# Kernel tuning notes

Hardware: AMD Instinct MI355X
Metric: run time of the kernel (lower is better)

Reference implementation:

```python
import jax, jax.numpy as jnp
import numpy as np

B, T_ENC, ENC_D = 32, 256, 512
T_DEC, MEL, R = 500, 80, 2
PRE = 256
ATTN_D, ATTN_RNN, DEC_RNN = 128, 1024, 1024
FILTERS, KSIZE = 32, 31
PAD = (KSIZE - 1) // 2


def setup_inputs() -> dict:
    key = jax.random.key(0)
    ks = jax.random.split(key, 32)
    n = lambda i, shape, s=0.05: jax.random.normal(ks[i], shape, dtype=jnp.float32) * s
    inp = {
        'encoder_outputs': jax.random.normal(ks[0], (B, T_ENC, ENC_D), dtype=jnp.float32),
        'inputs': jax.random.normal(ks[1], (B, T_DEC, MEL), dtype=jnp.float32),
        'memory_lengths': jax.random.randint(ks[2], (B,), T_ENC // 2, T_ENC + 1, dtype=jnp.int32),
        # prenet
        'W1': n(3, (PRE, MEL)), 'b1': jnp.zeros((PRE,), jnp.float32),
        'W2': n(4, (PRE, PRE)), 'b2': jnp.zeros((PRE,), jnp.float32),
        # memory layer
        'Wm': n(5, (ATTN_D, ENC_D)),
        # attention LSTMCell (input = PRE + ENC_D)
        'Wih_a': n(6, (4 * ATTN_RNN, PRE + ENC_D)), 'Whh_a': n(7, (4 * ATTN_RNN, ATTN_RNN)),
        'bih_a': jnp.zeros((4 * ATTN_RNN,), jnp.float32), 'bhh_a': jnp.zeros((4 * ATTN_RNN,), jnp.float32),
        # location-sensitive attention
        'Wq': n(8, (ATTN_D, ATTN_RNN)),
        'conv_w': n(9, (FILTERS, 1, KSIZE)), 'conv_b': jnp.zeros((FILTERS,), jnp.float32),
        'WL': n(10, (ATTN_D, FILTERS)),
        'v': n(11, (1, ATTN_D)),
        # decoder LSTMCell (input = ATTN_RNN + ENC_D)
        'Wih_d': n(12, (4 * DEC_RNN, ATTN_RNN + ENC_D)), 'Whh_d': n(13, (4 * DEC_RNN, DEC_RNN)),
        'bih_d': jnp.zeros((4 * DEC_RNN,), jnp.float32), 'bhh_d': jnp.zeros((4 * DEC_RNN,), jnp.float32),
        # projections (input = DEC_RNN + ENC_D)
        'Wmel': n(14, (MEL * R, DEC_RNN + ENC_D)), 'bmel': jnp.zeros((MEL * R,), jnp.float32),
        'Wstop': n(15, (1, DEC_RNN + ENC_D)), 'bstop': jnp.zeros((1,), jnp.float32),
    }
    return inp


def _lstm_cell(x, h, c, Wih, Whh, bih, bhh):
    gates = x @ Wih.T + bih + h @ Whh.T + bhh
    i, f, g, o = jnp.split(gates, 4, axis=-1)
    c = jax.nn.sigmoid(f) * c + jax.nn.sigmoid(i) * jnp.tanh(g)
    h = jax.nn.sigmoid(o) * jnp.tanh(c)
    return h, c


def _decoder(encoder_outputs, inputs, memory_lengths,
             W1, b1, W2, b2, Wm, Wih_a, Whh_a, bih_a, bhh_a,
             Wq, conv_w, conv_b, WL, v,
             Wih_d, Whh_d, bih_d, bhh_d, Wmel, bmel, Wstop, bstop):
    bsz = encoder_outputs.shape[0]
    t_enc = encoder_outputs.shape[1]
    processed_memory = encoder_outputs @ Wm.T  # (B, T_enc, attn_d)
    mask = jnp.arange(t_enc)[None, :] >= memory_lengths[:, None]  # True = padded

    n_steps = T_DEC // R
    # teacher-forced input frame per step: go frame, then last frame of each group
    tf = jnp.transpose(inputs[:, R - 1:T_DEC - 1:R, :], (1, 0, 2))  # (N-1, B, MEL)
    frames = jnp.concatenate([jnp.zeros((1, bsz, MEL), inputs.dtype), tf], axis=0)  # (N, B, MEL)

    def step(carry, frame):
        attn_h, attn_c, dec_h, dec_c, ctx, cum = carry
        # prenet (dropout disabled for deterministic reference / eval)
        x = jax.nn.relu(frame @ W1.T + b1)
        x = jax.nn.relu(x @ W2.T + b2)
        # attention LSTM cell
        attn_h, attn_c = _lstm_cell(jnp.concatenate([x, ctx], -1), attn_h, attn_c,
                                    Wih_a, Whh_a, bih_a, bhh_a)
        # location-sensitive energies
        pq = attn_h @ Wq.T  # (B, attn_d)
        loc = jax.lax.conv_general_dilated(
            cum[:, None, :], conv_w, window_strides=(1,), padding=[(PAD, PAD)],
            dimension_numbers=('NCH', 'OIH', 'NCH')) + conv_b[None, :, None]  # (B, F, T)
        ploc = jnp.transpose(loc, (0, 2, 1)) @ WL.T  # (B, T, attn_d)
        e = jnp.tanh(pq[:, None, :] + processed_memory + ploc) @ v[0]  # (B, T)
        e = jnp.where(mask, -1e9, e)
        align = jax.nn.softmax(e, axis=1)
        cum = cum + align
        ctx = jnp.einsum('bt,btd->bd', align, encoder_outputs)
        # decoder LSTM cell
        dec_h, dec_c = _lstm_cell(jnp.concatenate([attn_h, ctx], -1), dec_h, dec_c,
                                  Wih_d, Whh_d, bih_d, bhh_d)
        proj_in = jnp.concatenate([dec_h, ctx], -1)
        mel = (proj_in @ Wmel.T + bmel).reshape(bsz, R, MEL)
        stop = jax.nn.sigmoid(proj_in @ Wstop.T + bstop)  # (B, 1)
        return (attn_h, attn_c, dec_h, dec_c, ctx, cum), (mel, stop, align)

    z = lambda d: jnp.zeros((bsz, d), encoder_outputs.dtype)
    carry0 = (z(ATTN_RNN), z(ATTN_RNN), z(DEC_RNN), z(DEC_RNN), z(ENC_D),
              jnp.zeros((bsz, t_enc), encoder_outputs.dtype))
    _, (mels, stops, aligns) = jax.lax.scan(step, carry0, frames)
    mel_outputs = jnp.transpose(mels, (1, 0, 2, 3)).reshape(bsz, n_steps * R, MEL)
    stop_tokens = jnp.repeat(jnp.transpose(stops[:, :, 0]), R, axis=1)  # (B, N*R)
    attn_scores = jnp.transpose(aligns, (1, 0, 2))  # (B, N, T_enc)
    return mel_outputs, stop_tokens, attn_scores


def reference(encoder_outputs, inputs, memory_lengths,
              W1, b1, W2, b2, Wm, Wih_a, Whh_a, bih_a, bhh_a,
              Wq, conv_w, conv_b, WL, v,
              Wih_d, Whh_d, bih_d, bhh_d, Wmel, bmel, Wstop, bstop):
    return _decoder(encoder_outputs, inputs, memory_lengths,
                    W1, b1, W2, b2, Wm, Wih_a, Whh_a, bih_a, bhh_a,
                    Wq, conv_w, conv_b, WL, v,
                    Wih_d, Whh_d, bih_d, bhh_d, Wmel, bmel, Wstop, bstop)
```

## Files before the change

### kernel.cpp

```cpp
#include <hip/hip_runtime.h>
#include <cstdio>

static constexpr int cB = 32, cTENC = 256, cENCD = 512, cTDEC = 500, cMEL = 80,
    cNSTEP = 250, cPRE = 256, cAD = 128, cAR = 1024, cDR = 1024, cFLT = 32,
    cKSZ = 31, cPADC = 15, cNG = 4096;
static constexpr int cKA = cPRE + cENCD + cAR;
static constexpr int cKD = cAR + cENCD + cDR;
static constexpr int cKM = cDR + cENCD;
static constexpr int cNMP = 192;
static constexpr int cNSA = 14;
static constexpr int cNSD = 16;

typedef unsigned short ushortT;
typedef unsigned int uintT;
typedef unsigned long long ullT;

static constexpr size_t MEL_OFF = 0;
static constexpr size_t STOP_OFF = (size_t)cB * cTDEC * cMEL;
static constexpr size_t ATT_OFF = STOP_OFF + (size_t)cB * cTDEC;

static constexpr size_t WS_WATB = 0;
static constexpr size_t WS_WDTB = WS_WATB + (size_t)cKA * cNG / 2;
static constexpr size_t WS_WMT  = WS_WDTB + (size_t)cKD * cNG / 2;
static constexpr size_t WS_WQT  = WS_WMT  + (size_t)cKM * cNMP;
static constexpr size_t WS_WMTR = WS_WQT  + (size_t)cAR * cAD;
static constexpr size_t WS_PM   = WS_WMTR + (size_t)cENCD * cAD;
static constexpr size_t WS_XPRE = WS_PM   + (size_t)cB * cTENC * cAD;
static constexpr size_t WS_XA   = WS_XPRE + (size_t)cNSTEP * cPRE * cB;
static constexpr size_t WS_XD   = WS_XA   + (size_t)2 * cKA * cB;
static constexpr size_t WS_CA   = WS_XD   + (size_t)cKD * cB;
static constexpr size_t WS_CD   = WS_CA   + (size_t)cB * cAR;
static constexpr size_t WS_CUM  = WS_CD   + (size_t)cB * cDR;
static constexpr size_t WS_CTR  = WS_CUM  + (size_t)cB * cTENC;
static constexpr size_t WS_GA   = WS_CTR  + 16;
static constexpr size_t WS_GD   = WS_GA   + (size_t)cB * cNSA * cNG;
static constexpr size_t WS_PROJ = WS_GD   + (size_t)cB * cNSD * cNG;
static constexpr size_t WS_TOTAL = WS_PROJ + (size_t)cNSTEP * cKM * cB;
static constexpr size_t WS_X1   = WS_GA;

struct Args {
  const float *enc, *inputs;
  const int *mlen;
  const float *W1, *b1, *W2, *b2, *Wm;
  const float *Wih_a, *Whh_a, *bih_a, *bhh_a;
  const float *Wq, *conv_w, *conv_b, *WL, *v;
  const float *Wih_d, *Whh_d, *bih_d, *bhh_d;
  const float *Wmel, *bmel, *Wstop, *bstop;
  float *out;
  float *ws;
};

union SharedU {
  float xs[(160 + 8) * 32];
  struct {
    float h[cAR];
    float pq[cAD];
    float cumext[cTENC + 2 * cPADC];
    float eparts[2][cTENC];
    float e[cTENC];
    float sred[16];
    float loc[cFLT * 257];
    float wl[cAD * 33];
    float cw[cFLT * cKSZ];
    float vv[cAD];
  } attn;
  float melred[cB][164];
};

__device__ __forceinline__ float ld_sc(const float* p) {
  return __hip_atomic_load(p, __ATOMIC_RELAXED, __HIP_MEMORY_SCOPE_AGENT);
}
__device__ __forceinline__ void st_sc(float* p, float v) {
  __hip_atomic_store(p, v, __ATOMIC_RELAXED, __HIP_MEMORY_SCOPE_AGENT);
}
__device__ __forceinline__ float2 ld_sc2(const float2* p) {
  ullT u = __hip_atomic_load((const ullT*)p, __ATOMIC_RELAXED, __HIP_MEMORY_SCOPE_AGENT);
  float2 r;
  r.x = __uint_as_float((uintT)u);
  r.y = __uint_as_float((uintT)(u >> 32));
  return r;
}
__device__ __forceinline__ void st_sc2(float2* p, float x, float y) {
  ullT u = (ullT)__float_as_uint(x) | ((ullT)__float_as_uint(y) << 32);
  __hip_atomic_store((ullT*)p, u, __ATOMIC_RELAXED, __HIP_MEMORY_SCOPE_AGENT);
}

__device__ __forceinline__ void gbar(uintT* ctr, uintT target) {
  __syncthreads();
  if (threadIdx.x == 0) {
    __hip_atomic_fetch_add(ctr, 1u, __ATOMIC_RELAXED, __HIP_MEMORY_SCOPE_AGENT);
    while (__hip_atomic_load(ctr, __ATOMIC_RELAXED, __HIP_MEMORY_SCOPE_AGENT) < target) {
      __builtin_amdgcn_s_sleep(4);
    }
  }
  __syncthreads();
}

__device__ __forceinline__ float sigm_f(float x) { return 1.f / (1.f + __expf(-x)); }
__device__ __forceinline__ float tanh_f(float x) {
  float e = __expf(2.f * x);
  return 1.f - 2.f / (e + 1.f);
}

template <int KSPAN, int NS>
static __device__ void gemv_bf16(const ushortT* __restrict__ WT,
                                 const float* __restrict__ xT,
                                 float* __restrict__ part,
                                 int cb, int k0, int slot, float* __restrict__ xs) {
  const int tid = threadIdx.x;
  {
    const float2* src = (const float2*)(xT + (size_t)k0 * cB);
    float2* dst = (float2*)xs;
    for (int i = tid; i < KSPAN * 16; i += 512) dst[i] = ld_sc2(src + i);
  }
  __syncthreads();
  const int cq = tid & 63, bq = tid >> 6;
  const int col0 = cb * 512 + cq * 8;
  const ushortT* wp = WT + (size_t)k0 * cNG + col0;
  const float4* xp = (const float4*)xs + bq;
  float acc[8][4];
#pragma unroll
  for (int c = 0; c < 8; ++c)
#pragma unroll
    for (int j = 0; j < 4; ++j) acc[c][j] = 0.f;

  constexpr int PF = 8;
  uint4 wbuf[PF];
  float4 xbuf[PF];
#pragma unroll
  for (int i = 0; i < PF; ++i) {
    wbuf[i] = *(const uint4*)(wp + (size_t)i * cNG);
    xbuf[i] = xp[(size_t)i * 8];
  }
  for (int kb = 0; kb < KSPAN; kb += PF) {
#pragma unroll
    for (int i = 0; i < PF; ++i) {
      const uint4 w = wbuf[i];
      const float4 x4 = xbuf[i];
      const size_t kn = (size_t)(kb + i + PF);
      wbuf[i] = *(const uint4*)(wp + kn * cNG);
      xbuf[i] = xp[kn * 8];
      float wf[8];
      wf[0] = __uint_as_float(w.x << 16);
      wf[1] = __uint_as_float(w.x & 0xFFFF0000u);
      wf[2] = __uint_as_float(w.y << 16);
      wf[3] = __uint_as_float(w.y & 0xFFFF0000u);
      wf[4] = __uint_as_float(w.z << 16);
      wf[5] = __uint_as_float(w.z & 0xFFFF0000u);
      wf[6] = __uint_as_float(w.w << 16);
      wf[7] = __uint_as_float(w.w & 0xFFFF0000u);
      const float xv[4] = {x4.x, x4.y, x4.z, x4.w};
#pragma unroll
      for (int c = 0; c < 8; ++c)
#pragma unroll
        for (int j = 0; j < 4; ++j) acc[c][j] = fmaf(wf[c], xv[j], acc[c][j]);
    }
  }
  const int b0 = bq * 4;
#pragma unroll
  for (int j = 0; j < 4; ++j) {
    float2* dst = (float2*)&part[(((size_t)(b0 + j)) * NS + slot) * cNG + col0];
    st_sc2(dst + 0, acc[0][j], acc[1][j]);
    st_sc2(dst + 1, acc[2][j], acc[3][j]);
    st_sc2(dst + 2, acc[4][j], acc[5][j]);
    st_sc2(dst + 3, acc[6][j], acc[7][j]);
  }
  __syncthreads();
}

static __device__ void dec_cell(const Args& a, float* ws, int b, int s) {
  const int tid = threadIdx.x;
  const float* gd = ws + WS_GD + (size_t)b * cNSD * cNG;
  for (int h = tid; h < cDR; h += 512) {
    float g4[4];
#pragma unroll
    for (int gi = 0; gi < 4; ++gi) {
      const int n = gi * cDR + h;
      float sm = a.bih_d[n] + a.bhh_d[n];
#pragma unroll
      for (int p = 0; p < cNSD; ++p) sm += ld_sc(gd + (size_t)p * cNG + n);
      g4[gi] = sm;
    }
    const float co = ld_sc(ws + WS_CD + (size_t)b * cDR + h);
    const float cn = sigm_f(g4[1]) * co + sigm_f(g4[0]) * tanh_f(g4[2]);
    const float hn = sigm_f(g4[3]) * tanh_f(cn);
    st_sc(ws + WS_CD + (size_t)b * cDR + h, cn);
    st_sc(ws + WS_XD + (size_t)(cAR + cENCD + h) * cB + b, hn);
    st_sc(ws + WS_PROJ + ((size_t)s * cKM + h) * cB + b, hn);
  }
}

static __device__ void attn_wg(const Args& a, float* ws, int b, int t,
                               float* __restrict__ xa2, SharedU& sh) {
  const int tid = threadIdx.x;
  const float* ga = ws + WS_GA + (size_t)b * cNSA * cNG;
  for (int h = tid; h < cAR; h += 512) {
    float g4[4];
#pragma unroll
    for (int gi = 0; gi < 4; ++gi) {
      const int n = gi * cAR + h;
      float s = a.bih_a[n] + a.bhh_a[n];
#pragma unroll
      for (int p = 0; p < cNSA; ++p) s += ld_sc(ga + (size_t)p * cNG + n);
      g4[gi] = s;
    }
    const float co = ld_sc(ws + WS_CA + (size_t)b * cAR + h);
    const float cn = sigm_f(g4[1]) * co + sigm_f(g4[0]) * tanh_f(g4[2]);
    const float hn = sigm_f(g4[3]) * tanh_f(cn);
    st_sc(ws + WS_CA + (size_t)b * cAR + h, cn);
    sh.attn.h[h] = hn;
    st_sc(xa2 + (size_t)(cPRE + cENCD + h) * cB + b, hn);
    st_sc(ws + WS_XD + (size_t)h * cB + b, hn);
  }
  __syncthreads();
  {
    const int d = tid & 127, kc = tid >> 7;
    float acc = 0.f;
    const float* wq = ws + WS_WQT;
    const int k0 = kc * 256;
    for (int k = k0; k < k0 + 256; ++k) acc = fmaf(sh.attn.h[k], wq[(size_t)k * cAD + d], acc);
    sh.attn.loc[kc * 128 + d] = acc;
  }
  for (int i = tid; i < cAD * 33; i += 512) {
    const int dd = i / 33, f = i - dd * 33;
    sh.attn.wl[i] = (f < cFLT) ? a.WL[dd * cFLT + f] : 0.f;
  }
  for (int i = tid; i < cFLT * cKSZ; i += 512) sh.attn.cw[i] = a.conv_w[i];
  if (tid < cAD) sh.attn.vv[tid] = a.v[tid];
  if (tid < cTENC) sh.attn.cumext[cPADC + tid] = ld_sc(ws + WS_CUM + (size_t)b * cTENC + tid);
  if (tid < 2 * cPADC) sh.attn.cumext[tid < cPADC ? tid : cTENC + tid] = 0.f;
  __syncthreads();
  if (tid < cAD)
    sh.attn.pq[tid] = sh.attn.loc[tid] + sh.attn.loc[128 + tid] +
                      sh.attn.loc[256 + tid] + sh.attn.loc[384 + tid];
  __syncthreads();
  for (int i = tid; i < cFLT * cTENC; i += 512) {
    const int f = i >> 8, te = i & 255;
    float s = a.conv_b[f];
#pragma unroll
    for (int j = 0; j < cKSZ; ++j) s = fmaf(sh.attn.cumext[te + j], sh.attn.cw[f * cKSZ + j], s);
    sh.attn.loc[f * 257 + te] = s;
  }
  __syncthreads();
  {
    const int d = tid & 127, tq = tid >> 7, wv = tid >> 6;
    float wlr[cFLT];
#pragma unroll
    for (int f = 0; f < cFLT; ++f) wlr[f] = sh.attn.wl[d * 33 + f];
    const float pqd = sh.attn.pq[d], vd = sh.attn.vv[d];
    const float* pmb = ws + WS_PM + (size_t)b * cTENC * cAD;
    for (int tt = 0; tt < cTENC / 4; ++tt) {
      const int te = tt * 4 + tq;
      float s = pqd + pmb[(size_t)te * cAD + d];
#pragma unroll
      for (int f = 0; f < cFLT; ++f) s = fmaf(sh.attn.loc[f * 257 + te], wlr[f], s);
      float p = tanh_f(s) * vd;
#pragma unroll
      for (int off = 32; off > 0; off >>= 1) p += __shfl_xor(p, off, 64);
      if ((tid & 63) == 0) sh.attn.eparts[wv & 1][te] = p;
    }
  }
  __syncthreads();
  const int mlen = a.mlen[b];
  if (tid < cTENC) {
    float ev = sh.attn.eparts[0][tid] + sh.attn.eparts[1][tid];
    if (tid >= mlen) ev = -1e9f;
    sh.attn.e[tid] = ev;
  }
  __syncthreads();
  const int wv = tid >> 6;
  {
    float xv = sh.attn.e[tid & 255];
#pragma unroll
    for (int off = 32; off > 0; off >>= 1) xv = fmaxf(xv, __shfl_xor(xv, off, 64));
    if ((tid & 63) == 0) sh.attn.sred[wv] = xv;
  }
  __syncthreads();
  float m = sh.attn.sred[0];
#pragma unroll
  for (int i = 1; i < 8; ++i) m = fmaxf(m, sh.attn.sred[i]);
  const float pex = (tid < cTENC) ? __expf(sh.attn.e[tid] - m) : 0.f;
  {
    float sv = pex;
#pragma unroll
    for (int off = 32; off > 0; off >>= 1) sv += __shfl_xor(sv, off, 64);
    if ((tid & 63) == 0) sh.attn.sred[8 + wv] = sv;
  }
  __syncthreads();
  float ssum = 0.f;
#pragma unroll
  for (int i = 0; i < 8; ++i) ssum += sh.attn.sred[8 + i];
  const float rs = 1.f / ssum;
  if (tid < cTENC) {
    const float al = pex * rs;
    sh.attn.e[tid] = al;
    a.out[ATT_OFF + ((size_t)b * cNSTEP + t) * cTENC + tid] = al;
    st_sc(ws + WS_CUM + (size_t)b * cTENC + tid, sh.attn.cumext[cPADC + tid] + al);
  }
  __syncthreads();
  {
    const int k = tid;
    float acc = 0.f;
    const float* encb = a.enc + (size_t)b * cTENC * cENCD + k;
    for (int te = 0; te < cTENC; ++te) acc = fmaf(sh.attn.e[te], encb[(size_t)te * cENCD], acc);
    st_sc(xa2 + (size_t)(cPRE + k) * cB + b, acc);
    st_sc(ws + WS_XD + (size_t)(cAR + k) * cB + b, acc);
    st_sc(ws + WS_PROJ + ((size_t)t * cKM + cDR + k) * cB + b, acc);
  }
}

static __device__ void mel_proj(const Args& a, float* ws, SharedU& sh) {
  const int tid = threadIdx.x;
  const int c = tid & 255, sub = tid >> 8;
  for (int t = blockIdx.x; t < cNSTEP; t += gridDim.x) {
    float acc[cB];
#pragma unroll
    for (int b = 0; b < cB; ++b) acc[b] = 0.f;
    if (c < 161) {
      const float* wmt = ws + WS_WMT;
      const float* xr0 = ws + WS_PROJ + (size_t)t * cKM * cB;
      const int k0 = sub * 768;
      for (int k = k0; k < k0 + 768; ++k) {
        const float w = wmt[(size_t)k * cNMP + c];
        const float* xr = xr0 + (size_t)k * cB;
#pragma unroll
        for (int b = 0; b < cB; ++b) acc[b] = fmaf(w, ld_sc(xr + b), acc[b]);
      }
    }
    __syncthreads();
    if (sub == 1 && c < 161) {
#pragma unroll
      for (int b = 0; b < cB; ++b) sh.melred[b][c] = acc[b];
    }
    __syncthreads();
    if (sub == 0 && c < 161) {
      if (c < 160) {
        const int fr = c / 80, mm = c % 80;
        const float bm = a.bmel[c];
#pragma unroll
        for (int b = 0; b < cB; ++b) {
          const float val = acc[b] + sh.melred[b][c] + bm;
          a.out[MEL_OFF + ((size_t)b * cTDEC + (2 * t + fr)) * cMEL + mm] = val;
        }
      } else {
        const float bs = a.bstop[0];
#pragma unroll
        for (int b = 0; b < cB; ++b) {
          const float sp = sigm_f(acc[b] + sh.melred[b][c] + bs);
          a.out[STOP_OFF + (size_t)b * cTDEC + 2 * t] = sp;
          a.out[STOP_OFF + (size_t)b * cTDEC + 2 * t + 1] = sp;
        }
      }
    }
    __syncthreads();
  }
}

__device__ __forceinline__ ushortT f2b(float f) {
  const uintT u = __float_as_uint(f);
  return (ushortT)((u + 0x7FFFu + ((u >> 16) & 1u)) >> 16);
}

__global__ void k_transpose(const float* __restrict__ src, float* __restrict__ dst,
                            int N, int K, int dpitch) {
  __shared__ float tile[64][65];
  const int tkn = K >> 6;
  const int tk = blockIdx.x % tkn, tn = blockIdx.x / tkn;
  const int c = threadIdx.x & 63, r4 = threadIdx.x >> 6;
  const int n0 = tn << 6, k0 = tk << 6;
#pragma unroll
  for (int rr = 0; rr < 16; ++rr) {
    const int r = r4 * 16 + rr;
    tile[r][c] = src[(size_t)(n0 + r) * K + k0 + c];
  }
  __syncthreads();
#pragma unroll
  for (int rr = 0; rr < 16; ++rr) {
    const int r = r4 * 16 + rr;
    dst[(size_t)(k0 + r) * dpitch + n0 + c] = tile[c][r];
  }
}

__global__ void k_transpose_b16(const float* __restrict__ src, ushortT* __restrict__ dst,
                                int N, int K, int dpitch) {
  __shared__ float tile[64][65];
  const int tkn = K >> 6;
  const int tk = blockIdx.x % tkn, tn = blockIdx.x / tkn;
  const int c = threadIdx.x & 63, r4 = threadIdx.x >> 6;
  const int n0 = tn << 6, k0 = tk << 6;
#pragma unroll
  for (int rr = 0; rr < 16; ++rr) {
    const int r = r4 * 16 + rr;
    tile[r][c] = src[(size_t)(n0 + r) * K + k0 + c];
  }
  __syncthreads();
#pragma unroll
  for (int rr = 0; rr < 16; ++rr) {
    const int r = r4 * 16 + rr;
    dst[(size_t)(k0 + r) * dpitch + n0 + c] = f2b(tile[c][r]);
  }
}

__global__ void k_prep_small(Args a) {
  const size_t i = (size_t)blockIdx.x * blockDim.x + threadIdx.x;
  if (i < 16) ((uintT*)(a.ws + WS_CTR))[i] = 0u;
  if (i >= (size_t)cKM * cNMP) return;
  const int k = (int)(i / cNMP), c = (int)(i % cNMP);
  a.ws[WS_WMT + i] = (c < 160) ? a.Wmel[(size_t)c * cKM + k]
                               : (c == 160 ? a.Wstop[k] : 0.f);
}

__global__ void k_prenet1(Args a) {
  const size_t i = (size_t)blockIdx.x * blockDim.x + threadIdx.x;
  if (i >= (size_t)cNSTEP * cB * cPRE) return;
  const int j = i & 255, b = (i >> 8) & 31, n = (int)(i >> 13);
  float acc = a.b1[j];
  if (n > 0) {
    const float* fr = a.inputs + ((size_t)b * cTDEC + (2 * n - 1)) * cMEL;
    for (int k = 0; k < cMEL; ++k) acc = fmaf(fr[k], a.W1[j * cMEL + k], acc);
  }
  a.ws[WS_X1 + i] = fmaxf(acc, 0.f);
}

__global__ void k_prenet2(Args a) {
  const size_t i = (size_t)blockIdx.x * blockDim.x + threadIdx.x;
  if (i >= (size_t)cNSTEP * cPRE * cB) return;
  const int b = i & 31, j = (i >> 5) & 255, n = (int)(i >> 13);
  float acc = a.b2[j];
  const float* x1 = a.ws + WS_X1 + ((size_t)n * cB + b) * cPRE;
  for (int k = 0; k < cPRE; ++k) acc = fmaf(x1[k], a.W2[j * cPRE + k], acc);
  a.ws[WS_XPRE + i] = fmaxf(acc, 0.f);
}

__global__ void k_pm(Args a) {
  const size_t i = (size_t)blockIdx.x * blockDim.x + threadIdx.x;
  if (i >= (size_t)cB * cTENC * cAD) return;
  const int d = i & 127, tt = (i >> 7) & 255, b = (int)(i >> 15);
  float acc = 0.f;
  const float* er = a.enc + ((size_t)b * cTENC + tt) * cENCD;
  const float* wt = a.ws + WS_WMTR;
  for (int k = 0; k < cENCD; ++k) acc = fmaf(er[k], wt[(size_t)k * cAD + d], acc);
  a.ws[WS_PM + i] = acc;
}

__global__ void __launch_bounds__(512, 1) k_loop(Args a) {
  __shared__ SharedU sh;
  float* ws = a.ws;
  uintT* ctr = (uintT*)(ws + WS_CTR);
  const ushortT* watb = (const ushortT*)(ws + WS_WATB);
  const ushortT* wdtb = (const ushortT*)(ws + WS_WDTB);
  const int wg = blockIdx.x;
  const int tid = threadIdx.x;
  uintT ph = 0;

  float* xa0 = ws + WS_XA;
  if (wg < 32) {
    const int b = wg;
    for (int i = tid; i < cTENC; i += 512) st_sc(ws + WS_CUM + (size_t)b * cTENC + i, 0.f);
    for (int i = tid; i < cAR; i += 512) st_sc(ws + WS_CA + (size_t)b * cAR + i, 0.f);
  } else if (wg < 64) {
    const int b = wg - 32;
    for (int i = tid; i < cDR; i += 512) st_sc(ws + WS_CD + (size_t)b * cDR + i, 0.f);
  } else if (wg < 80) {
    const int i = (wg - 64) * 512 + tid;
    st_sc(xa0 + i, ld_sc(ws + WS_XPRE + i));
  } else if (wg < 176) {
    const int i = (wg - 80) * 512 + tid;
    st_sc(xa0 + (size_t)cPRE * cB + i, 0.f);
  } else if (wg < 240) {
    const int i = (wg - 176) * 512 + tid;
    st_sc(ws + WS_XD + (size_t)(cAR + cENCD) * cB + i, 0.f);
  }
  ++ph; gbar(ctr, ph * 256u);

  for (int t = 0; t <= cNSTEP; ++t) {
    const float* xa = ws + WS_XA + (size_t)(t & 1) * cKA * cB;
    float* xa2 = ws + WS_XA + (size_t)((t + 1) & 1) * cKA * cB;
    if (wg < 112) {
      if (t < cNSTEP) {
        const int s = wg >> 3, cb = wg & 7;
        gemv_bf16<128, cNSA>(watb, xa, ws + WS_GA, cb, s * 128, s, sh.xs);
      }
    } else if (wg < 240) {
      if (t >= 1) {
        const int i = wg - 112, s = i >> 3, cb = i & 7;
        gemv_bf16<160, cNSD>(wdtb, ws + WS_XD, ws + WS_GD, cb, s * 160, s, sh.xs);
      }
    }
    ++ph; gbar(ctr, ph * 256u);
    if (wg < 32) {
      if (t < cNSTEP) attn_wg(a, ws, wg, t, xa2, sh);
    } else if (wg < 64) {
      if (t >= 1) dec_cell(a, ws, wg - 32, t - 1);
    } else if (wg < 80) {
      if (t + 1 < cNSTEP) {
        const int i = (wg - 64) * 512 + tid;
        st_sc(xa2 + i, ld_sc(ws + WS_XPRE + (size_t)(t + 1) * cPRE * cB + i));
      }
    }
    ++ph; gbar(ctr, ph * 256u);
  }
  mel_proj(a, ws, sh);
}

extern "C" void kernel_launch(void* const* d_in, const int* in_sizes, int n_in,
                              void* d_out, int out_size, void* d_ws, size_t ws_size,
                              hipStream_t stream) {
  (void)in_sizes; (void)n_in; (void)out_size;
  Args a;
  a.enc = (const float*)d_in[0];
  a.inputs = (const float*)d_in[1];
  a.mlen = (const int*)d_in[2];
  a.W1 = (const float*)d_in[3];  a.b1 = (const float*)d_in[4];
  a.W2 = (const float*)d_in[5];  a.b2 = (const float*)d_in[6];
  a.Wm = (const float*)d_in[7];
  a.Wih_a = (const float*)d_in[8];  a.Whh_a = (const float*)d_in[9];
  a.bih_a = (const float*)d_in[10]; a.bhh_a = (const float*)d_in[11];
  a.Wq = (const float*)d_in[12];
  a.conv_w = (const float*)d_in[13]; a.conv_b = (const float*)d_in[14];
  a.WL = (const float*)d_in[15];     a.v = (const float*)d_in[16];
  a.Wih_d = (const float*)d_in[17];  a.Whh_d = (const float*)d_in[18];
  a.bih_d = (const float*)d_in[19];  a.bhh_d = (const float*)d_in[20];
  a.Wmel = (const float*)d_in[21];   a.bmel = (const float*)d_in[22];
  a.Wstop = (const float*)d_in[23];  a.bstop = (const float*)d_in[24];
  a.out = (float*)d_out;
  a.ws = (float*)d_ws;

  if (ws_size < WS_TOTAL * sizeof(float)) {
    fprintf(stderr, "kernel_launch: ws too small: need %zu bytes, have %zu\n",
            WS_TOTAL * sizeof(float), ws_size);
    return;
  }

  float* ws = a.ws;
  ushortT* watb = (ushortT*)(ws + WS_WATB);
  ushortT* wdtb = (ushortT*)(ws + WS_WDTB);
  k_transpose_b16<<<dim3((768 / 64) * (4096 / 64)), dim3(256), 0, stream>>>(
      a.Wih_a, watb, 4096, 768, cNG);
  k_transpose_b16<<<dim3((1024 / 64) * (4096 / 64)), dim3(256), 0, stream>>>(
      a.Whh_a, watb + (size_t)768 * cNG, 4096, 1024, cNG);
  k_transpose_b16<<<dim3((1536 / 64) * (4096 / 64)), dim3(256), 0, stream>>>(
      a.Wih_d, wdtb, 4096, 1536, cNG);
  k_transpose_b16<<<dim3((1024 / 64) * (4096 / 64)), dim3(256), 0, stream>>>(
      a.Whh_d, wdtb + (size_t)1536 * cNG, 4096, 1024, cNG);
  k_transpose<<<dim3((1024 / 64) * (128 / 64)), dim3(256), 0, stream>>>(
      a.Wq, ws + WS_WQT, 128, 1024, cAD);
  k_transpose<<<dim3((512 / 64) * (128 / 64)), dim3(256), 0, stream>>>(
      a.Wm, ws + WS_WMTR, 128, 512, cAD);

  k_prep_small<<<dim3((cKM * cNMP + 255) / 256), dim3(256), 0, stream>>>(a);
  k_prenet1<<<dim3(8000), dim3(256), 0, stream>>>(a);
  k_prenet2<<<dim3(8000), dim3(256), 0, stream>>>(a);
  k_pm<<<dim3(4096), dim3(256), 0, stream>>>(a);

  void* params[] = { (void*)&a };
  hipError_t err = hipLaunchCooperativeKernel((const void*)k_loop, dim3(256), dim3(512),
                                              params, 0, stream);
  if (err != hipSuccess) {
    fprintf(stderr, "kernel_launch: cooperative launch failed: %s\n",
            hipGetErrorString(err));
  }
}
```

Before: 39.10 ms.

## Keep per-block LSTM weight slices resident in LDS across all decoder steps

Each GEMV block now loads its bf16 weight slice (128 or 132 rows × 512 columns) into dynamic shared memory once, then reuses it for all 250 steps. Only the few extra decoder rows are streamed from global memory. This removes the per-step global re-read of the LSTM weights. Activation buffers change to batch-major layout, attention moves to blocks 240-255 (each handles two batch rows), and the global barrier is split across 8 padded counters to reduce atomic contention. The cost is about 158KB of LDS per block and serialized attention work on 16 blocks.

```diff
diff --git a/kernel.cpp b/kernel.cpp
--- a/kernel.cpp
+++ b/kernel.cpp
@@ -10,6 +10,9 @@
 static constexpr int cNMP = 192;
 static constexpr int cNSA = 14;
 static constexpr int cNSD = 16;
+static constexpr int cRDA = 128;
+static constexpr int cRDD = 132;
+static constexpr int cDYN = 158208;
 
 typedef unsigned short ushortT;
 typedef unsigned int uintT;
@@ -32,7 +35,7 @@
 static constexpr size_t WS_CD   = WS_CA   + (size_t)cB * cAR;
 static constexpr size_t WS_CUM  = WS_CD   + (size_t)cB * cDR;
 static constexpr size_t WS_CTR  = WS_CUM  + (size_t)cB * cTENC;
-static constexpr size_t WS_GA   = WS_CTR  + 16;
+static constexpr size_t WS_GA   = WS_CTR  + 128;
 static constexpr size_t WS_GD   = WS_GA   + (size_t)cB * cNSA * cNG;
 static constexpr size_t WS_PROJ = WS_GD   + (size_t)cB * cNSD * cNG;
 static constexpr size_t WS_TOTAL = WS_PROJ + (size_t)cNSTEP * cKM * cB;
@@ -50,21 +53,17 @@
   float *ws;
 };
 
-union SharedU {
-  float xs[(160 + 8) * 32];
-  struct {
-    float h[cAR];
-    float pq[cAD];
-    float cumext[cTENC + 2 * cPADC];
-    float eparts[2][cTENC];
-    float e[cTENC];
-    float sred[16];
-    float loc[cFLT * 257];
-    float wl[cAD * 33];
-    float cw[cFLT * cKSZ];
-    float vv[cAD];
-  } attn;
-  float melred[cB][164];
+struct AttnSh {
+  float h[cAR];
+  float pq[cAD];
+  float cumext[cTENC + 2 * cPADC];
+  float eparts[2][cTENC];
+  float e[cTENC];
+  float sred[16];
+  float loc[cFLT * 257];
+  float wl[cAD * 33];
+  float cw[cFLT * cKSZ];
+  float vv[cAD];
 };
 
 __device__ __forceinline__ float ld_sc(const float* p) {
@@ -72,26 +71,22 @@
 }
 __device__ __forceinline__ void st_sc(float* p, float v) {
   __hip_atomic_store(p, v, __ATOMIC_RELAXED, __HIP_MEMORY_SCOPE_AGENT);
-}
-__device__ __forceinline__ float2 ld_sc2(const float2* p) {
-  ullT u = __hip_atomic_load((const ullT*)p, __ATOMIC_RELAXED, __HIP_MEMORY_SCOPE_AGENT);
-  float2 r;
-  r.x = __uint_as_float((uintT)u);
-  r.y = __uint_as_float((uintT)(u >> 32));
-  return r;
 }
 __device__ __forceinline__ void st_sc2(float2* p, float x, float y) {
   ullT u = (ullT)__float_as_uint(x) | ((ullT)__float_as_uint(y) << 32);
   __hip_atomic_store((ullT*)p, u, __ATOMIC_RELAXED, __HIP_MEMORY_SCOPE_AGENT);
 }
 
-__device__ __forceinline__ void gbar(uintT* ctr, uintT target) {
-  __syncthreads();
-  if (threadIdx.x == 0) {
-    __hip_atomic_fetch_add(ctr, 1u, __ATOMIC_RELAXED, __HIP_MEMORY_SCOPE_AGENT);
-    while (__hip_atomic_load(ctr, __ATOMIC_RELAXED, __HIP_MEMORY_SCOPE_AGENT) < target) {
-      __builtin_amdgcn_s_sleep(4);
-    }
+__device__ __forceinline__ void gbar(uintT* ctrs, uintT ph) {
+  __syncthreads();
+  if (threadIdx.x == 0)
+    __hip_atomic_fetch_add(ctrs + (blockIdx.x & 7) * 16, 1u,
+                           __ATOMIC_RELAXED, __HIP_MEMORY_SCOPE_AGENT);
+  if (threadIdx.x < 8) {
+    const uintT target = ph * 32u;
+    while (__hip_atomic_load(ctrs + threadIdx.x * 16, __ATOMIC_RELAXED,
+                             __HIP_MEMORY_SCOPE_AGENT) < target)
+      __builtin_amdgcn_s_sleep(8);
   }
   __syncthreads();
 }
@@ -102,70 +97,76 @@
   return 1.f - 2.f / (e + 1.f);
 }
 
-template <int KSPAN, int NS>
-static __device__ void gemv_bf16(const ushortT* __restrict__ WT,
-                                 const float* __restrict__ xT,
-                                 float* __restrict__ part,
-                                 int cb, int k0, int slot, float* __restrict__ xs) {
+__device__ __forceinline__ void fma8x4(float (&acc)[8][4], const uint4 w, const float4 x4) {
+  float wf[8];
+  wf[0] = __uint_as_float(w.x << 16);
+  wf[1] = __uint_as_float(w.x & 0xFFFF0000u);
+  wf[2] = __uint_as_float(w.y << 16);
+  wf[3] = __uint_as_float(w.y & 0xFFFF0000u);
+  wf[4] = __uint_as_float(w.z << 16);
+  wf[5] = __uint_as_float(w.z & 0xFFFF0000u);
+  wf[6] = __uint_as_float(w.w << 16);
+  wf[7] = __uint_as_float(w.w & 0xFFFF0000u);
+  const float xv[4] = {x4.x, x4.y, x4.z, x4.w};
+#pragma unroll
+  for (int c = 0; c < 8; ++c)
+#pragma unroll
+    for (int j = 0; j < 4; ++j) acc[c][j] = fmaf(wf[c], xv[j], acc[c][j]);
+}
+
+static __device__ void preload_w(uint4* dst, const ushortT* src, int rows) {
+  const int tid = threadIdx.x;
+  for (int i = tid; i < rows * 64; i += 512) {
+    const int r = i >> 6, u = i & 63;
+    dst[i] = *(const uint4*)(src + (size_t)r * cNG + u * 8);
+  }
+}
+
+template <int KSPAN, int RD, int NS>
+static __device__ void gemv_lds(const ushortT* __restrict__ wlds,
+                                const ushortT* __restrict__ wstream,
+                                const float* __restrict__ xT, int xstride,
+                                float* __restrict__ part,
+                                int col0, int slot, float* __restrict__ xs) {
   const int tid = threadIdx.x;
   {
-    const float2* src = (const float2*)(xT + (size_t)k0 * cB);
-    float2* dst = (float2*)xs;
-    for (int i = tid; i < KSPAN * 16; i += 512) dst[i] = ld_sc2(src + i);
+    const int b = tid >> 4, kt = tid & 15;
+    const float* src = xT + (size_t)b * xstride;
+    for (int k = kt; k < KSPAN; k += 16) xs[k * 36 + b] = ld_sc(src + k);
   }
   __syncthreads();
   const int cq = tid & 63, bq = tid >> 6;
-  const int col0 = cb * 512 + cq * 8;
-  const ushortT* wp = WT + (size_t)k0 * cNG + col0;
-  const float4* xp = (const float4*)xs + bq;
+  const ushortT* wl = wlds + cq * 8;
+  const float* xp = xs + bq * 4;
   float acc[8][4];
 #pragma unroll
   for (int c = 0; c < 8; ++c)
 #pragma unroll
     for (int j = 0; j < 4; ++j) acc[c][j] = 0.f;
-
-  constexpr int PF = 8;
-  uint4 wbuf[PF];
-  float4 xbuf[PF];
-#pragma unroll
-  for (int i = 0; i < PF; ++i) {
-    wbuf[i] = *(const uint4*)(wp + (size_t)i * cNG);
-    xbuf[i] = xp[(size_t)i * 8];
-  }
-  for (int kb = 0; kb < KSPAN; kb += PF) {
-#pragma unroll
-    for (int i = 0; i < PF; ++i) {
-      const uint4 w = wbuf[i];
-      const float4 x4 = xbuf[i];
-      const size_t kn = (size_t)(kb + i + PF);
-      wbuf[i] = *(const uint4*)(wp + kn * cNG);
-      xbuf[i] = xp[kn * 8];
-      float wf[8];
-      wf[0] = __uint_as_float(w.x << 16);
-      wf[1] = __uint_as_float(w.x & 0xFFFF0000u);
-      wf[2] = __uint_as_float(w.y << 16);
-      wf[3] = __uint_as_float(w.y & 0xFFFF0000u);
-      wf[4] = __uint_as_float(w.z << 16);
-      wf[5] = __uint_as_float(w.z & 0xFFFF0000u);
-      wf[6] = __uint_as_float(w.w << 16);
-      wf[7] = __uint_as_float(w.w & 0xFFFF0000u);
-      const float xv[4] = {x4.x, x4.y, x4.z, x4.w};
-#pragma unroll
-      for (int c = 0; c < 8; ++c)
-#pragma unroll
-        for (int j = 0; j < 4; ++j) acc[c][j] = fmaf(wf[c], xv[j], acc[c][j]);
+#pragma unroll 4
+  for (int k = 0; k < RD; ++k) {
+    const uint4 w = *(const uint4*)(wl + (size_t)k * 512);
+    const float4 x4 = *(const float4*)(xp + k * 36);
+    fma8x4(acc, w, x4);
+  }
+  if (RD < KSPAN) {
+    const ushortT* wg2 = wstream + cq * 8;
+#pragma unroll 4
+    for (int k = RD; k < KSPAN; ++k) {
+      const uint4 w = *(const uint4*)(wg2 + (size_t)k * cNG);
+      const float4 x4 = *(const float4*)(xp + k * 36);
+      fma8x4(acc, w, x4);
     }
   }
   const int b0 = bq * 4;
 #pragma unroll
   for (int j = 0; j < 4; ++j) {
-    float2* dst = (float2*)&part[(((size_t)(b0 + j)) * NS + slot) * cNG + col0];
+    float2* dst = (float2*)&part[(((size_t)(b0 + j)) * NS + slot) * cNG + col0 + cq * 8];
     st_sc2(dst + 0, acc[0][j], acc[1][j]);
     st_sc2(dst + 1, acc[2][j], acc[3][j]);
     st_sc2(dst + 2, acc[4][j], acc[5][j]);
     st_sc2(dst + 3, acc[6][j], acc[7][j]);
   }
-  __syncthreads();
 }
 
 static __device__ void dec_cell(const Args& a, float* ws, int b, int s) {
@@ -185,13 +186,13 @@
     const float cn = sigm_f(g4[1]) * co + sigm_f(g4[0]) * tanh_f(g4[2]);
     const float hn = sigm_f(g4[3]) * tanh_f(cn);
     st_sc(ws + WS_CD + (size_t)b * cDR + h, cn);
-    st_sc(ws + WS_XD + (size_t)(cAR + cENCD + h) * cB + b, hn);
-    st_sc(ws + WS_PROJ + ((size_t)s * cKM + h) * cB + b, hn);
+    st_sc(ws + WS_XD + (size_t)b * cKD + (cAR + cENCD) + h, hn);
+    st_sc(ws + WS_PROJ + ((size_t)s * cB + b) * cKM + h, hn);
   }
 }
 
 static __device__ void attn_wg(const Args& a, float* ws, int b, int t,
-                               float* __restrict__ xa2, SharedU& sh) {
+                               float* __restrict__ xa2, AttnSh& sh) {
   const int tid = threadIdx.x;
   const float* ga = ws + WS_GA + (size_t)b * cNSA * cNG;
   for (int h = tid; h < cAR; h += 512) {
@@ -208,9 +209,9 @@
     const float cn = sigm_f(g4[1]) * co + sigm_f(g4[0]) * tanh_f(g4[2]);
     const float hn = sigm_f(g4[3]) * tanh_f(cn);
     st_sc(ws + WS_CA + (size_t)b * cAR + h, cn);
-    sh.attn.h[h] = hn;
-    st_sc(xa2 + (size_t)(cPRE + cENCD + h) * cB + b, hn);
-    st_sc(ws + WS_XD + (size_t)h * cB + b, hn);
+    sh.h[h] = hn;
+    st_sc(xa2 + (size_t)b * cKA + (cPRE + cENCD) + h, hn);
+    st_sc(ws + WS_XD + (size_t)b * cKD + h, hn);
   }
   __syncthreads();
   {
@@ -218,98 +219,98 @@
     float acc = 0.f;
     const float* wq = ws + WS_WQT;
     const int k0 = kc * 256;
-    for (int k = k0; k < k0 + 256; ++k) acc = fmaf(sh.attn.h[k], wq[(size_t)k * cAD + d], acc);
-    sh.attn.loc[kc * 128 + d] = acc;
+    for (int k = k0; k < k0 + 256; ++k) acc = fmaf(sh.h[k], wq[(size_t)k * cAD + d], acc);
+    sh.loc[kc * 128 + d] = acc;
   }
   for (int i = tid; i < cAD * 33; i += 512) {
     const int dd = i / 33, f = i - dd * 33;
-    sh.attn.wl[i] = (f < cFLT) ? a.WL[dd * cFLT + f] : 0.f;
-  }
-  for (int i = tid; i < cFLT * cKSZ; i += 512) sh.attn.cw[i] = a.conv_w[i];
-  if (tid < cAD) sh.attn.vv[tid] = a.v[tid];
-  if (tid < cTENC) sh.attn.cumext[cPADC + tid] = ld_sc(ws + WS_CUM + (size_t)b * cTENC + tid);
-  if (tid < 2 * cPADC) sh.attn.cumext[tid < cPADC ? tid : cTENC + tid] = 0.f;
+    sh.wl[i] = (f < cFLT) ? a.WL[dd * cFLT + f] : 0.f;
+  }
+  for (int i = tid; i < cFLT * cKSZ; i += 512) sh.cw[i] = a.conv_w[i];
+  if (tid < cAD) sh.vv[tid] = a.v[tid];
+  if (tid < cTENC) sh.cumext[cPADC + tid] = ld_sc(ws + WS_CUM + (size_t)b * cTENC + tid);
+  if (tid < 2 * cPADC) sh.cumext[tid < cPADC ? tid : cTENC + tid] = 0.f;
   __syncthreads();
   if (tid < cAD)
-    sh.attn.pq[tid] = sh.attn.loc[tid] + sh.attn.loc[128 + tid] +
-                      sh.attn.loc[256 + tid] + sh.attn.loc[384 + tid];
+    sh.pq[tid] = sh.loc[tid] + sh.loc[128 + tid] + sh.loc[256 + tid] + sh.loc[384 + tid];
   __syncthreads();
   for (int i = tid; i < cFLT * cTENC; i += 512) {
     const int f = i >> 8, te = i & 255;
     float s = a.conv_b[f];
 #pragma unroll
-    for (int j = 0; j < cKSZ; ++j) s = fmaf(sh.attn.cumext[te + j], sh.attn.cw[f * cKSZ + j], s);
-    sh.attn.loc[f * 257 + te] = s;
+    for (int j = 0; j < cKSZ; ++j) s = fmaf(sh.cumext[te + j], sh.cw[f * cKSZ + j], s);
+    sh.loc[f * 257 + te] = s;
   }
   __syncthreads();
   {
     const int d = tid & 127, tq = tid >> 7, wv = tid >> 6;
     float wlr[cFLT];
 #pragma unroll
-    for (int f = 0; f < cFLT; ++f) wlr[f] = sh.attn.wl[d * 33 + f];
-    const float pqd = sh.attn.pq[d], vd = sh.attn.vv[d];
+    for (int f = 0; f < cFLT; ++f) wlr[f] = sh.wl[d * 33 + f];
+    const float pqd = sh.pq[d], vd = sh.vv[d];
     const float* pmb = ws + WS_PM + (size_t)b * cTENC * cAD;
     for (int tt = 0; tt < cTENC / 4; ++tt) {
       const int te = tt * 4 + tq;
       float s = pqd + pmb[(size_t)te * cAD + d];
 #pragma unroll
-      for (int f = 0; f < cFLT; ++f) s = fmaf(sh.attn.loc[f * 257 + te], wlr[f], s);
+      for (int f = 0; f < cFLT; ++f) s = fmaf(sh.loc[f * 257 + te], wlr[f], s);
       float p = tanh_f(s) * vd;
 #pragma unroll
       for (int off = 32; off > 0; off >>= 1) p += __shfl_xor(p, off, 64);
-      if ((tid & 63) == 0) sh.attn.eparts[wv & 1][te] = p;
+      if ((tid & 63) == 0) sh.eparts[wv & 1][te] = p;
     }
   }
   __syncthreads();
   const int mlen = a.mlen[b];
   if (tid < cTENC) {
-    float ev = sh.attn.eparts[0][tid] + sh.attn.eparts[1][tid];
+    float ev = sh.eparts[0][tid] + sh.eparts[1][tid];
     if (tid >= mlen) ev = -1e9f;
-    sh.attn.e[tid] = ev;
+    sh.e[tid] = ev;
   }
   __syncthreads();
   const int wv = tid >> 6;
   {
-    float xv = sh.attn.e[tid & 255];
+    float xv = sh.e[tid & 255];
 #pragma unroll
     for (int off = 32; off > 0; off >>= 1) xv = fmaxf(xv, __shfl_xor(xv, off, 64));
-    if ((tid & 63) == 0) sh.attn.sred[wv] = xv;
-  }
-  __syncthreads();
-  float m = sh.attn.sred[0];
-#pragma unroll
-  for (int i = 1; i < 8; ++i) m = fmaxf(m, sh.attn.sred[i]);
-  const float pex = (tid < cTENC) ? __expf(sh.attn.e[tid] - m) : 0.f;
+    if ((tid & 63) == 0) sh.sred[wv] = xv;
+  }
+  __syncthreads();
+  float m = sh.sred[0];
+#pragma unroll
+  for (int i = 1; i < 8; ++i) m = fmaxf(m, sh.sred[i]);
+  const float pex = (tid < cTENC) ? __expf(sh.e[tid] - m) : 0.f;
   {
     float sv = pex;
 #pragma unroll
     for (int off = 32; off > 0; off >>= 1) sv += __shfl_xor(sv, off, 64);
-    if ((tid & 63) == 0) sh.attn.sred[8 + wv] = sv;
+    if ((tid & 63) == 0) sh.sred[8 + wv] = sv;
   }
   __syncthreads();
   float ssum = 0.f;
 #pragma unroll
-  for (int i = 0; i < 8; ++i) ssum += sh.attn.sred[8 + i];
+  for (int i = 0; i < 8; ++i) ssum += sh.sred[8 + i];
   const float rs = 1.f / ssum;
   if (tid < cTENC) {
     const float al = pex * rs;
-    sh.attn.e[tid] = al;
+    sh.e[tid] = al;
     a.out[ATT_OFF + ((size_t)b * cNSTEP + t) * cTENC + tid] = al;
-    st_sc(ws + WS_CUM + (size_t)b * cTENC + tid, sh.attn.cumext[cPADC + tid] + al);
+    st_sc(ws + WS_CUM + (size_t)b * cTENC + tid, sh.cumext[cPADC + tid] + al);
   }
   __syncthreads();
   {
     const int k = tid;
     float acc = 0.f;
     const float* encb = a.enc + (size_t)b * cTENC * cENCD + k;
-    for (int te = 0; te < cTENC; ++te) acc = fmaf(sh.attn.e[te], encb[(size_t)te * cENCD], acc);
-    st_sc(xa2 + (size_t)(cPRE + k) * cB + b, acc);
-    st_sc(ws + WS_XD + (size_t)(cAR + k) * cB + b, acc);
-    st_sc(ws + WS_PROJ + ((size_t)t * cKM + cDR + k) * cB + b, acc);
-  }
-}
-
-static __device__ void mel_proj(const Args& a, float* ws, SharedU& sh) {
+    for (int te = 0; te < cTENC; ++te) acc = fmaf(sh.e[te], encb[(size_t)te * cENCD], acc);
+    st_sc(xa2 + (size_t)b * cKA + cPRE + k, acc);
+    st_sc(ws + WS_XD + (size_t)b * cKD + cAR + k, acc);
+    st_sc(ws + WS_PROJ + ((size_t)t * cB + b) * cKM + cDR + k, acc);
+  }
+  __syncthreads();
+}
+
+static __device__ void mel_proj(const Args& a, float* ws, float* melred) {
   const int tid = threadIdx.x;
   const int c = tid & 255, sub = tid >> 8;
   for (int t = blockIdx.x; t < cNSTEP; t += gridDim.x) {
@@ -318,19 +319,18 @@
     for (int b = 0; b < cB; ++b) acc[b] = 0.f;
     if (c < 161) {
       const float* wmt = ws + WS_WMT;
-      const float* xr0 = ws + WS_PROJ + (size_t)t * cKM * cB;
+      const float* xr0 = ws + WS_PROJ + (size_t)t * cB * cKM;
       const int k0 = sub * 768;
       for (int k = k0; k < k0 + 768; ++k) {
         const float w = wmt[(size_t)k * cNMP + c];
-        const float* xr = xr0 + (size_t)k * cB;
-#pragma unroll
-        for (int b = 0; b < cB; ++b) acc[b] = fmaf(w, ld_sc(xr + b), acc[b]);
+#pragma unroll
+        for (int b = 0; b < cB; ++b) acc[b] = fmaf(w, xr0[(size_t)b * cKM + k], acc[b]);
       }
     }
     __syncthreads();
     if (sub == 1 && c < 161) {
 #pragma unroll
-      for (int b = 0; b < cB; ++b) sh.melred[b][c] = acc[b];
+      for (int b = 0; b < cB; ++b) melred[b * 164 + c] = acc[b];
     }
     __syncthreads();
     if (sub == 0 && c < 161) {
@@ -339,14 +339,14 @@
         const float bm = a.bmel[c];
 #pragma unroll
         for (int b = 0; b < cB; ++b) {
-          const float val = acc[b] + sh.melred[b][c] + bm;
+          const float val = acc[b] + melred[b * 164 + c] + bm;
           a.out[MEL_OFF + ((size_t)b * cTDEC + (2 * t + fr)) * cMEL + mm] = val;
         }
       } else {
         const float bs = a.bstop[0];
 #pragma unroll
         for (int b = 0; b < cB; ++b) {
-          const float sp = sigm_f(acc[b] + sh.melred[b][c] + bs);
+          const float sp = sigm_f(acc[b] + melred[b * 164 + c] + bs);
           a.out[STOP_OFF + (size_t)b * cTDEC + 2 * t] = sp;
           a.out[STOP_OFF + (size_t)b * cTDEC + 2 * t + 1] = sp;
         }
@@ -403,7 +403,7 @@
 
 __global__ void k_prep_small(Args a) {
   const size_t i = (size_t)blockIdx.x * blockDim.x + threadIdx.x;
-  if (i < 16) ((uintT*)(a.ws + WS_CTR))[i] = 0u;
+  if (i < 128) ((uintT*)(a.ws + WS_CTR))[i] = 0u;
   if (i >= (size_t)cKM * cNMP) return;
   const int k = (int)(i / cNMP), c = (int)(i % cNMP);
   a.ws[WS_WMT + i] = (c < 160) ? a.Wmel[(size_t)c * cKM + k]
@@ -425,11 +425,11 @@
 __global__ void k_prenet2(Args a) {
   const size_t i = (size_t)blockIdx.x * blockDim.x + threadIdx.x;
   if (i >= (size_t)cNSTEP * cPRE * cB) return;
-  const int b = i & 31, j = (i >> 5) & 255, n = (int)(i >> 13);
+  const int j = i & 255, b = (i >> 8) & 31, n = (int)(i >> 13);
   float acc = a.b2[j];
   const float* x1 = a.ws + WS_X1 + ((size_t)n * cB + b) * cPRE;
   for (int k = 0; k < cPRE; ++k) acc = fmaf(x1[k], a.W2[j * cPRE + k], acc);
-  a.ws[WS_XPRE + i] = fmaxf(acc, 0.f);
+  a.ws[WS_XPRE + ((size_t)n * cB + b) * cPRE + j] = fmaxf(acc, 0.f);
 }
 
 __global__ void k_pm(Args a) {
@@ -444,15 +444,32 @@
 }
 
 __global__ void __launch_bounds__(512, 1) k_loop(Args a) {
-  __shared__ SharedU sh;
+  extern __shared__ char dyn[];
   float* ws = a.ws;
-  uintT* ctr = (uintT*)(ws + WS_CTR);
+  uintT* ctrs = (uintT*)(ws + WS_CTR);
   const ushortT* watb = (const ushortT*)(ws + WS_WATB);
   const ushortT* wdtb = (const ushortT*)(ws + WS_WDTB);
   const int wg = blockIdx.x;
   const int tid = threadIdx.x;
   uintT ph = 0;
 
+  ushortT* wlds = (ushortT*)dyn;
+  AttnSh* at = (AttnSh*)dyn;
+  float* melred = (float*)dyn;
+
+  const int iA = wg, sA = iA >> 3, cbA = iA & 7;
+  const int iD = wg - 112, sD = iD >> 3, cbD = iD & 7;
+  const int col0A = cbA * 512, k0A = sA * 128;
+  const int col0D = cbD * 512, k0D = sD * 160;
+  float* xsA = (float*)(dyn + cRDA * 1024);
+  float* xsD = (float*)(dyn + cRDD * 1024);
+  const ushortT* wstrD = wdtb + (size_t)k0D * cNG + col0D;
+
+  if (wg < 112) {
+    preload_w((uint4*)wlds, watb + (size_t)k0A * cNG + col0A, cRDA);
+  } else if (wg < 240) {
+    preload_w((uint4*)wlds, wstrD, cRDD);
+  }
   float* xa0 = ws + WS_XA;
   if (wg < 32) {
     const int b = wg;
@@ -463,44 +480,50 @@
     for (int i = tid; i < cDR; i += 512) st_sc(ws + WS_CD + (size_t)b * cDR + i, 0.f);
   } else if (wg < 80) {
     const int i = (wg - 64) * 512 + tid;
-    st_sc(xa0 + i, ld_sc(ws + WS_XPRE + i));
+    const int b = i >> 8, j = i & 255;
+    st_sc(xa0 + (size_t)b * cKA + j, ws[WS_XPRE + i]);
   } else if (wg < 176) {
     const int i = (wg - 80) * 512 + tid;
-    st_sc(xa0 + (size_t)cPRE * cB + i, 0.f);
+    const int b = i / 1536, j = i % 1536;
+    st_sc(xa0 + (size_t)b * cKA + cPRE + j, 0.f);
   } else if (wg < 240) {
     const int i = (wg - 176) * 512 + tid;
-    st_sc(ws + WS_XD + (size_t)(cAR + cENCD) * cB + i, 0.f);
-  }
-  ++ph; gbar(ctr, ph * 256u);
+    const int b = i >> 10, h = i & 1023;
+    st_sc(ws + WS_XD + (size_t)b * cKD + (cAR + cENCD) + h, 0.f);
+  }
+  ++ph; gbar(ctrs, ph);
 
   for (int t = 0; t <= cNSTEP; ++t) {
     const float* xa = ws + WS_XA + (size_t)(t & 1) * cKA * cB;
     float* xa2 = ws + WS_XA + (size_t)((t + 1) & 1) * cKA * cB;
     if (wg < 112) {
+      if (t < cNSTEP)
+        gemv_lds<128, cRDA, cNSA>(wlds, nullptr, xa + k0A, cKA,
+                                  ws + WS_GA, col0A, sA, xsA);
+    } else if (wg < 240) {
+      if (t >= 1)
+        gemv_lds<160, cRDD, cNSD>(wlds, wstrD, ws + WS_XD + k0D, cKD,
+                                  ws + WS_GD, col0D, sD, xsD);
+    }
+    ++ph; gbar(ctrs, ph);
+    if (wg >= 240) {
       if (t < cNSTEP) {
-        const int s = wg >> 3, cb = wg & 7;
-        gemv_bf16<128, cNSA>(watb, xa, ws + WS_GA, cb, s * 128, s, sh.xs);
+        attn_wg(a, ws, wg - 240, t, xa2, *at);
+        attn_wg(a, ws, wg - 240 + 16, t, xa2, *at);
       }
-    } else if (wg < 240) {
-      if (t >= 1) {
-        const int i = wg - 112, s = i >> 3, cb = i & 7;
-        gemv_bf16<160, cNSD>(wdtb, ws + WS_XD, ws + WS_GD, cb, s * 160, s, sh.xs);
-      }
-    }
-    ++ph; gbar(ctr, ph * 256u);
-    if (wg < 32) {
-      if (t < cNSTEP) attn_wg(a, ws, wg, t, xa2, sh);
-    } else if (wg < 64) {
+    } else if (wg >= 32 && wg < 64) {
       if (t >= 1) dec_cell(a, ws, wg - 32, t - 1);
-    } else if (wg < 80) {
+    } else if (wg >= 64 && wg < 80) {
       if (t + 1 < cNSTEP) {
         const int i = (wg - 64) * 512 + tid;
-        st_sc(xa2 + i, ld_sc(ws + WS_XPRE + (size_t)(t + 1) * cPRE * cB + i));
+        const int b = i >> 8, j = i & 255;
+        st_sc(xa2 + (size_t)b * cKA + j,
+              ws[WS_XPRE + (size_t)(t + 1) * cPRE * cB + i]);
       }
     }
-    ++ph; gbar(ctr, ph * 256u);
-  }
-  mel_proj(a, ws, sh);
+    ++ph; gbar(ctrs, ph);
+  }
+  mel_proj(a, ws, melred);
 }
 
 extern "C" void kernel_launch(void* const* d_in, const int* in_sizes, int n_in,
@@ -553,9 +576,14 @@
   k_prenet2<<<dim3(8000), dim3(256), 0, stream>>>(a);
   k_pm<<<dim3(4096), dim3(256), 0, stream>>>(a);
 
+  hipError_t e0 = hipFuncSetAttribute((const void*)k_loop,
+                                      hipFuncAttributeMaxDynamicSharedMemorySize, cDYN);
+  if (e0 != hipSuccess)
+    fprintf(stderr, "kernel_launch: setattr failed: %s\n", hipGetErrorString(e0));
+
   void* params[] = { (void*)&a };
   hipError_t err = hipLaunchCooperativeKernel((const void*)k_loop, dim3(256), dim3(512),
-                                              params, 0, stream);
+                                              params, cDYN, stream);
   if (err != hipSuccess) {
     fprintf(stderr, "kernel_launch: cooperative launch failed: %s\n",
             hipGetErrorString(err));
```

Result: slower. 63.28 ms (+61.9%).
